# Kernel tuning notes

Measured on AMD Instinct MI355X. Metric: run time of the kernel, lower is better.

## Reference

```python
import jax, jax.numpy as jnp
import numpy as np

B, N_IN, O, IN_L, OUT_L = 256, 1152, 10, 8, 16
ITERS = 3
EPS = 1e-7

def squash(s, eps):
    # norm over the capsule-length axis (-2), keepdim, as in the torch code
    dot = jnp.sum(s * s, axis=-2, keepdims=True)
    return (dot / (1.0 + dot) / jnp.sqrt(dot + eps)) * s

def setup_inputs() -> dict:
    key = jax.random.key(0)
    k1, k2, k3 = jax.random.split(key, 3)
    x = jax.random.normal(k1, (B, N_IN, IN_L, 1), dtype=jnp.float32)
    weight = 0.05 * jax.random.normal(k2, (1, N_IN, O, IN_L, OUT_L), dtype=jnp.float32)
    bias = 0.05 * jax.random.normal(k3, (1, 1, O, OUT_L, 1), dtype=jnp.float32)
    return {"x": x, "weight": weight, "bias": bias}

def reference(x, weight, bias):
    # u_hat[b,n,o,k] = sum_i W[0,n,o,i,k] * x[b,n,i,0]  -> (B, N, O, K, 1)
    u_hat = jnp.einsum('noik,bni->bnok', weight[0], x[..., 0])[..., None]
    u_det = jax.lax.stop_gradient(u_hat)
    b_ij = jnp.zeros((x.shape[0], N_IN, O, 1, 1), dtype=x.dtype)
    v = None
    for r in range(ITERS):
        c = jax.nn.softmax(b_ij, axis=2)          # routing coefficients over out caps
        u = u_hat if r == ITERS - 1 else u_det    # detached except last iter
        s = jnp.sum(c * u, axis=1, keepdims=True) + bias  # (B,1,O,K,1)
        v = squash(s, EPS)
        if r != ITERS - 1:
            # agreement: sum over capsule-length axis 3 -> (B,N,O,1,1)
            b_ij = b_ij + jnp.sum(u_det * v, axis=3, keepdims=True)
    return v
```

## Files before the change

kernel.cpp:

```cpp
#include <hip/hip_runtime.h>
#include <hip/hip_bf16.h>

#define BB   256
#define NIN  1152
#define OO   10
#define IL   8
#define OL   16
#define ROW  (OO*OL)
#define EPSQ 1e-7f

typedef unsigned short ushx8 __attribute__((ext_vector_type(8)));
typedef unsigned short ushx4 __attribute__((ext_vector_type(4)));

__device__ __forceinline__ float bf2f(unsigned short h) {
    unsigned u = ((unsigned)h) << 16;
    return __builtin_bit_cast(float, u);
}

__global__ __launch_bounds__(320, 1) void caps_build(
    const float* __restrict__ x, const float* __restrict__ w,
    unsigned short* __restrict__ u)
{
    const int t  = threadIdx.x;
    const int nl = t / 20;
    const int s  = t - nl * 20;
    const int o  = s >> 1;
    const int k8 = s & 1;
    const int n  = blockIdx.x * 16 + nl;
    const int b0 = blockIdx.y * 32;

    const float* wb = w + (size_t)n * (OO * IL * OL) + (o * IL) * OL + k8 * 8;
    float wr[IL][8];
    #pragma unroll
    for (int i = 0; i < IL; ++i) {
        const float4 wa = *reinterpret_cast<const float4*>(wb + i * OL);
        const float4 wc = *reinterpret_cast<const float4*>(wb + i * OL + 4);
        wr[i][0] = wa.x; wr[i][1] = wa.y; wr[i][2] = wa.z; wr[i][3] = wa.w;
        wr[i][4] = wc.x; wr[i][5] = wc.y; wr[i][6] = wc.z; wr[i][7] = wc.w;
    }

    const float4* xb = reinterpret_cast<const float4*>(x + ((size_t)b0 * NIN + n) * IL);
    unsigned short* ub = u + ((size_t)b0 * NIN + n) * ROW + o * OL + k8 * 8;

    #pragma unroll 4
    for (int bl = 0; bl < 32; ++bl) {
        const float4 xa = xb[(size_t)bl * (NIN * 2)];
        const float4 xc = xb[(size_t)bl * (NIN * 2) + 1];
        const float xv[IL] = {xa.x, xa.y, xa.z, xa.w, xc.x, xc.y, xc.z, xc.w};

        float uv[8];
        #pragma unroll
        for (int j = 0; j < 8; ++j) {
            float acc = wr[0][j] * xv[0];
            #pragma unroll
            for (int i = 1; i < IL; ++i) acc = fmaf(wr[i][j], xv[i], acc);
            uv[j] = acc;
        }

        union { ushx8 v; __hip_bfloat162 h[4]; } pk;
        #pragma unroll
        for (int j = 0; j < 4; ++j)
            pk.h[j] = __float22bfloat162_rn(make_float2(uv[2 * j], uv[2 * j + 1]));
        *reinterpret_cast<ushx8*>(ub + (size_t)bl * ((size_t)NIN * ROW)) = pk.v;
    }
}

__global__ __launch_bounds__(512) void caps_route(
    const unsigned short* __restrict__ u, const float* __restrict__ vsum,
    const float* __restrict__ bias, const float* __restrict__ prevAdd,
    float* __restrict__ outv, float scale)
{
    __shared__ float lds[8][ROW];
    const int t = threadIdx.x;
    const int q = t & 3;
    const int g = t >> 2;
    const int b = blockIdx.x;
    const int wv = t >> 6;

    float4 sp[OO];
    #pragma unroll
    for (int o = 0; o < OO; ++o) sp[o] = make_float4(0.f, 0.f, 0.f, 0.f);

    const unsigned short* ub = u + (size_t)b * NIN * ROW + (q << 2);

    if (vsum == nullptr) {
        for (int m = 0; m < 9; ++m) {
            const unsigned short* un = ub + (size_t)(g + (m << 7)) * ROW;
            #pragma unroll
            for (int o = 0; o < OO; ++o) {
                const ushx4 raw = *reinterpret_cast<const ushx4*>(un + o * OL);
                sp[o].x += bf2f(raw[0]);
                sp[o].y += bf2f(raw[1]);
                sp[o].z += bf2f(raw[2]);
                sp[o].w += bf2f(raw[3]);
            }
        }
    } else {
        float4 vs[OO];
        #pragma unroll
        for (int o = 0; o < OO; ++o)
            vs[o] = *reinterpret_cast<const float4*>(vsum + (size_t)b * ROW + o * OL + q * 4);

        for (int m = 0; m < 9; ++m) {
            const unsigned short* un = ub + (size_t)(g + (m << 7)) * ROW;
            ushx4 raw[OO];
            #pragma unroll
            for (int o = 0; o < OO; ++o)
                raw[o] = *reinterpret_cast<const ushx4*>(un + o * OL);

            float bij[OO];
            #pragma unroll
            for (int o = 0; o < OO; ++o) {
                float d = bf2f(raw[o][0]) * vs[o].x;
                d = fmaf(bf2f(raw[o][1]), vs[o].y, d);
                d = fmaf(bf2f(raw[o][2]), vs[o].z, d);
                d = fmaf(bf2f(raw[o][3]), vs[o].w, d);
                d += __shfl_xor(d, 1, 4);
                d += __shfl_xor(d, 2, 4);
                bij[o] = d;
            }
            float mx = bij[0];
            #pragma unroll
            for (int o = 1; o < OO; ++o) mx = fmaxf(mx, bij[o]);
            float e[OO], se = 0.f;
            #pragma unroll
            for (int o = 0; o < OO; ++o) { e[o] = __expf(bij[o] - mx); se += e[o]; }
            const float r = 1.f / se;
            #pragma unroll
            for (int o = 0; o < OO; ++o) {
                const float c = e[o] * r;
                sp[o].x = fmaf(c, bf2f(raw[o][0]), sp[o].x);
                sp[o].y = fmaf(c, bf2f(raw[o][1]), sp[o].y);
                sp[o].z = fmaf(c, bf2f(raw[o][2]), sp[o].z);
                sp[o].w = fmaf(c, bf2f(raw[o][3]), sp[o].w);
            }
        }
    }

    #pragma unroll
    for (int o = 0; o < OO; ++o) {
        #pragma unroll
        for (int msk = 4; msk <= 32; msk <<= 1) {
            sp[o].x += __shfl_xor(sp[o].x, msk);
            sp[o].y += __shfl_xor(sp[o].y, msk);
            sp[o].z += __shfl_xor(sp[o].z, msk);
            sp[o].w += __shfl_xor(sp[o].w, msk);
        }
    }
    if ((t & 63) < 4) {
        #pragma unroll
        for (int o = 0; o < OO; ++o) {
            lds[wv][o * OL + q * 4 + 0] = sp[o].x;
            lds[wv][o * OL + q * 4 + 1] = sp[o].y;
            lds[wv][o * OL + q * 4 + 2] = sp[o].z;
            lds[wv][o * OL + q * 4 + 3] = sp[o].w;
        }
    }
    __syncthreads();

    if (t < ROW) {
        float ssum = 0.f;
        #pragma unroll
        for (int wvi = 0; wvi < 8; ++wvi) ssum += lds[wvi][t];
        const float sv = scale * ssum + bias[t];

        float d = sv * sv;
        d += __shfl_xor(d, 1, 16);
        d += __shfl_xor(d, 2, 16);
        d += __shfl_xor(d, 4, 16);
        d += __shfl_xor(d, 8, 16);
        const float f = d / ((1.f + d) * sqrtf(d + EPSQ));
        float v = f * sv;
        if (prevAdd) v += prevAdd[(size_t)b * ROW + t];
        outv[(size_t)b * ROW + t] = v;
    }
}

extern "C" void kernel_launch(void* const* d_in, const int* in_sizes, int n_in,
                              void* d_out, int out_size, void* d_ws, size_t ws_size,
                              hipStream_t stream) {
    const float* x    = (const float*)d_in[0];
    const float* w    = (const float*)d_in[1];
    const float* bias = (const float*)d_in[2];
    float* out = (float*)d_out;

    unsigned short* u = (unsigned short*)d_ws;
    float* v0  = (float*)((char*)d_ws + (size_t)BB * NIN * ROW * 2);
    float* vsb = v0 + (size_t)BB * ROW;

    caps_build<<<dim3(NIN / 16, BB / 32), 320, 0, stream>>>(x, w, u);
    caps_route<<<BB, 512, 0, stream>>>(u, nullptr, bias, nullptr, v0, 0.1f);
    caps_route<<<BB, 512, 0, stream>>>(u, v0, bias, v0, vsb, 1.0f);
    caps_route<<<BB, 512, 0, stream>>>(u, vsb, bias, nullptr, out, 1.0f);
}
```

Measured before the change: 92.36 us.

## Fuse three routing iterations into one kernel and stage build inputs in LDS

Replaces the three separate routing launches with a single 768-thread kernel per batch that loops over the iterations, keeping v in shared memory instead of round-tripping it through global memory. The build kernel now stages weights (with an XOR swizzle) and x tiles in LDS, uses smaller 8-capsule blocks, and computes two batch rows per step. This is meant to remove launch overhead and global v traffic, and to improve reuse in the build phase. In exchange it adds extra block-wide barriers and relies on the re-read of u across iterations being served by cache.

After: 87.58 us. 5.2% less time.

```diff
diff --git a/kernel.cpp b/kernel.cpp
--- a/kernel.cpp
+++ b/kernel.cpp
@@ -8,6 +8,8 @@
 #define OL   16
 #define ROW  (OO*OL)
 #define EPSQ 1e-7f
+#define NT   8
+#define BT   32
 
 typedef unsigned short ushx8 __attribute__((ext_vector_type(8)));
 typedef unsigned short ushx4 __attribute__((ext_vector_type(4)));
@@ -17,162 +19,195 @@
     return __builtin_bit_cast(float, u);
 }
 
-__global__ __launch_bounds__(320, 1) void caps_build(
+__global__ __launch_bounds__(160) void caps_build(
     const float* __restrict__ x, const float* __restrict__ w,
     unsigned short* __restrict__ u)
 {
+    __shared__ float4 wl4[NT][321];
+    __shared__ float4 xl4[BT * 16];
     const int t  = threadIdx.x;
+    const int n0 = blockIdx.x * NT;
+    const int b0 = blockIdx.y * BT;
+
+    const float4* wg = reinterpret_cast<const float4*>(w) + (size_t)n0 * 320;
+    for (int j = t; j < NT * 320; j += 160) {
+        const int row = j / 320;
+        const int lin = j - row * 320;
+        const int o   = lin >> 5;
+        const int rem = lin & 31;
+        const int i   = rem >> 2;
+        const int kh  = rem & 3;
+        const int ip  = i ^ (o & 1);
+        wl4[row][(o << 5) | (ip << 2) | kh] = wg[j];
+    }
+    const float4* xg = reinterpret_cast<const float4*>(x);
+    for (int j = t; j < BT * 16; j += 160) {
+        const int bl = j >> 4;
+        const int r  = j & 15;
+        xl4[j] = xg[((size_t)(b0 + bl) * NIN + n0) * 2 + r];
+    }
+    __syncthreads();
+
     const int nl = t / 20;
     const int s  = t - nl * 20;
     const int o  = s >> 1;
     const int k8 = s & 1;
-    const int n  = blockIdx.x * 16 + nl;
-    const int b0 = blockIdx.y * 32;
-
-    const float* wb = w + (size_t)n * (OO * IL * OL) + (o * IL) * OL + k8 * 8;
-    float wr[IL][8];
+    const int p  = o & 1;
+    const float4* wbase = &wl4[nl][(o << 5) | (k8 << 1)];
+    const float4* xbase = &xl4[nl * 2];
+    unsigned short* ub = u + ((size_t)b0 * NIN + n0 + nl) * ROW + o * OL + k8 * 8;
+    const size_t ustride = (size_t)NIN * ROW;
+
+    for (int bl = 0; bl < BT; bl += 2) {
+        const float4 xa0 = xbase[bl * 16];
+        const float4 xa1 = xbase[bl * 16 + 1];
+        const float4 xb0 = xbase[bl * 16 + 16];
+        const float4 xb1 = xbase[bl * 16 + 17];
+        const float xv0[IL] = {xa0.x, xa0.y, xa0.z, xa0.w, xa1.x, xa1.y, xa1.z, xa1.w};
+        const float xv1[IL] = {xb0.x, xb0.y, xb0.z, xb0.w, xb1.x, xb1.y, xb1.z, xb1.w};
+
+        float a0[8] = {0,0,0,0,0,0,0,0};
+        float a1[8] = {0,0,0,0,0,0,0,0};
+        #pragma unroll
+        for (int i = 0; i < IL; ++i) {
+            const float4 wlo = wbase[(i ^ p) << 2];
+            const float4 whi = wbase[((i ^ p) << 2) | 1];
+            const float wv[8] = {wlo.x, wlo.y, wlo.z, wlo.w, whi.x, whi.y, whi.z, whi.w};
+            #pragma unroll
+            for (int j = 0; j < 8; ++j) {
+                a0[j] = fmaf(wv[j], xv0[i], a0[j]);
+                a1[j] = fmaf(wv[j], xv1[i], a1[j]);
+            }
+        }
+        union { ushx8 v; __hip_bfloat162 h[4]; } p0, p1;
+        #pragma unroll
+        for (int j = 0; j < 4; ++j) {
+            p0.h[j] = __float22bfloat162_rn(make_float2(a0[2*j], a0[2*j+1]));
+            p1.h[j] = __float22bfloat162_rn(make_float2(a1[2*j], a1[2*j+1]));
+        }
+        *reinterpret_cast<ushx8*>(ub + (size_t)bl * ustride)       = p0.v;
+        *reinterpret_cast<ushx8*>(ub + (size_t)(bl + 1) * ustride) = p1.v;
+    }
+}
+
+__global__ __launch_bounds__(768) void caps_route3(
+    const unsigned short* __restrict__ u, const float* __restrict__ bias,
+    float* __restrict__ outv)
+{
+    __shared__ float lds[12][ROW];
+    __shared__ float vbuf[ROW];
+    const int t  = threadIdx.x;
+    const int q  = t & 3;
+    const int g  = t >> 2;
+    const int wv = t >> 6;
+    const int b  = blockIdx.x;
+    const unsigned short* ub = u + (size_t)b * NIN * ROW + (q << 2);
+
+    float bsv = 0.f;
+    if (t < ROW) bsv = bias[t];
+    float vprev = 0.f;
+
+    float4 sp[OO];
+
     #pragma unroll
-    for (int i = 0; i < IL; ++i) {
-        const float4 wa = *reinterpret_cast<const float4*>(wb + i * OL);
-        const float4 wc = *reinterpret_cast<const float4*>(wb + i * OL + 4);
-        wr[i][0] = wa.x; wr[i][1] = wa.y; wr[i][2] = wa.z; wr[i][3] = wa.w;
-        wr[i][4] = wc.x; wr[i][5] = wc.y; wr[i][6] = wc.z; wr[i][7] = wc.w;
-    }
-
-    const float4* xb = reinterpret_cast<const float4*>(x + ((size_t)b0 * NIN + n) * IL);
-    unsigned short* ub = u + ((size_t)b0 * NIN + n) * ROW + o * OL + k8 * 8;
-
-    #pragma unroll 4
-    for (int bl = 0; bl < 32; ++bl) {
-        const float4 xa = xb[(size_t)bl * (NIN * 2)];
-        const float4 xc = xb[(size_t)bl * (NIN * 2) + 1];
-        const float xv[IL] = {xa.x, xa.y, xa.z, xa.w, xc.x, xc.y, xc.z, xc.w};
-
-        float uv[8];
-        #pragma unroll
-        for (int j = 0; j < 8; ++j) {
-            float acc = wr[0][j] * xv[0];
-            #pragma unroll
-            for (int i = 1; i < IL; ++i) acc = fmaf(wr[i][j], xv[i], acc);
-            uv[j] = acc;
-        }
-
-        union { ushx8 v; __hip_bfloat162 h[4]; } pk;
-        #pragma unroll
-        for (int j = 0; j < 4; ++j)
-            pk.h[j] = __float22bfloat162_rn(make_float2(uv[2 * j], uv[2 * j + 1]));
-        *reinterpret_cast<ushx8*>(ub + (size_t)bl * ((size_t)NIN * ROW)) = pk.v;
-    }
-}
-
-__global__ __launch_bounds__(512) void caps_route(
-    const unsigned short* __restrict__ u, const float* __restrict__ vsum,
-    const float* __restrict__ bias, const float* __restrict__ prevAdd,
-    float* __restrict__ outv, float scale)
-{
-    __shared__ float lds[8][ROW];
-    const int t = threadIdx.x;
-    const int q = t & 3;
-    const int g = t >> 2;
-    const int b = blockIdx.x;
-    const int wv = t >> 6;
-
-    float4 sp[OO];
-    #pragma unroll
-    for (int o = 0; o < OO; ++o) sp[o] = make_float4(0.f, 0.f, 0.f, 0.f);
-
-    const unsigned short* ub = u + (size_t)b * NIN * ROW + (q << 2);
-
-    if (vsum == nullptr) {
-        for (int m = 0; m < 9; ++m) {
-            const unsigned short* un = ub + (size_t)(g + (m << 7)) * ROW;
+    for (int iter = 0; iter < 3; ++iter) {
+        #pragma unroll
+        for (int o = 0; o < OO; ++o) sp[o] = make_float4(0.f, 0.f, 0.f, 0.f);
+
+        if (iter == 0) {
+            for (int m = 0; m < 6; ++m) {
+                const unsigned short* un = ub + (size_t)(g + m * 192) * ROW;
+                #pragma unroll
+                for (int o = 0; o < OO; ++o) {
+                    const ushx4 raw = *reinterpret_cast<const ushx4*>(un + o * OL);
+                    sp[o].x += bf2f(raw[0]);
+                    sp[o].y += bf2f(raw[1]);
+                    sp[o].z += bf2f(raw[2]);
+                    sp[o].w += bf2f(raw[3]);
+                }
+            }
+        } else {
+            float4 vs[OO];
+            #pragma unroll
+            for (int o = 0; o < OO; ++o)
+                vs[o] = *reinterpret_cast<const float4*>(&vbuf[o * OL + (q << 2)]);
+
+            for (int m = 0; m < 6; ++m) {
+                const unsigned short* un = ub + (size_t)(g + m * 192) * ROW;
+                ushx4 raw[OO];
+                #pragma unroll
+                for (int o = 0; o < OO; ++o)
+                    raw[o] = *reinterpret_cast<const ushx4*>(un + o * OL);
+
+                float bij[OO];
+                #pragma unroll
+                for (int o = 0; o < OO; ++o) {
+                    float d = bf2f(raw[o][0]) * vs[o].x;
+                    d = fmaf(bf2f(raw[o][1]), vs[o].y, d);
+                    d = fmaf(bf2f(raw[o][2]), vs[o].z, d);
+                    d = fmaf(bf2f(raw[o][3]), vs[o].w, d);
+                    d += __shfl_xor(d, 1, 4);
+                    d += __shfl_xor(d, 2, 4);
+                    bij[o] = d;
+                }
+                float mx = bij[0];
+                #pragma unroll
+                for (int o = 1; o < OO; ++o) mx = fmaxf(mx, bij[o]);
+                float e[OO], se = 0.f;
+                #pragma unroll
+                for (int o = 0; o < OO; ++o) { e[o] = __expf(bij[o] - mx); se += e[o]; }
+                const float r = 1.f / se;
+                #pragma unroll
+                for (int o = 0; o < OO; ++o) {
+                    const float c = e[o] * r;
+                    sp[o].x = fmaf(c, bf2f(raw[o][0]), sp[o].x);
+                    sp[o].y = fmaf(c, bf2f(raw[o][1]), sp[o].y);
+                    sp[o].z = fmaf(c, bf2f(raw[o][2]), sp[o].z);
+                    sp[o].w = fmaf(c, bf2f(raw[o][3]), sp[o].w);
+                }
+            }
+        }
+
+        #pragma unroll
+        for (int o = 0; o < OO; ++o) {
+            #pragma unroll
+            for (int msk = 4; msk <= 32; msk <<= 1) {
+                sp[o].x += __shfl_xor(sp[o].x, msk);
+                sp[o].y += __shfl_xor(sp[o].y, msk);
+                sp[o].z += __shfl_xor(sp[o].z, msk);
+                sp[o].w += __shfl_xor(sp[o].w, msk);
+            }
+        }
+        if ((t & 63) < 4) {
             #pragma unroll
             for (int o = 0; o < OO; ++o) {
-                const ushx4 raw = *reinterpret_cast<const ushx4*>(un + o * OL);
-                sp[o].x += bf2f(raw[0]);
-                sp[o].y += bf2f(raw[1]);
-                sp[o].z += bf2f(raw[2]);
-                sp[o].w += bf2f(raw[3]);
-            }
-        }
-    } else {
-        float4 vs[OO];
-        #pragma unroll
-        for (int o = 0; o < OO; ++o)
-            vs[o] = *reinterpret_cast<const float4*>(vsum + (size_t)b * ROW + o * OL + q * 4);
-
-        for (int m = 0; m < 9; ++m) {
-            const unsigned short* un = ub + (size_t)(g + (m << 7)) * ROW;
-            ushx4 raw[OO];
-            #pragma unroll
-            for (int o = 0; o < OO; ++o)
-                raw[o] = *reinterpret_cast<const ushx4*>(un + o * OL);
-
-            float bij[OO];
-            #pragma unroll
-            for (int o = 0; o < OO; ++o) {
-                float d = bf2f(raw[o][0]) * vs[o].x;
-                d = fmaf(bf2f(raw[o][1]), vs[o].y, d);
-                d = fmaf(bf2f(raw[o][2]), vs[o].z, d);
-                d = fmaf(bf2f(raw[o][3]), vs[o].w, d);
-                d += __shfl_xor(d, 1, 4);
-                d += __shfl_xor(d, 2, 4);
-                bij[o] = d;
-            }
-            float mx = bij[0];
-            #pragma unroll
-            for (int o = 1; o < OO; ++o) mx = fmaxf(mx, bij[o]);
-            float e[OO], se = 0.f;
-            #pragma unroll
-            for (int o = 0; o < OO; ++o) { e[o] = __expf(bij[o] - mx); se += e[o]; }
-            const float r = 1.f / se;
-            #pragma unroll
-            for (int o = 0; o < OO; ++o) {
-                const float c = e[o] * r;
-                sp[o].x = fmaf(c, bf2f(raw[o][0]), sp[o].x);
-                sp[o].y = fmaf(c, bf2f(raw[o][1]), sp[o].y);
-                sp[o].z = fmaf(c, bf2f(raw[o][2]), sp[o].z);
-                sp[o].w = fmaf(c, bf2f(raw[o][3]), sp[o].w);
-            }
-        }
-    }
-
-    #pragma unroll
-    for (int o = 0; o < OO; ++o) {
-        #pragma unroll
-        for (int msk = 4; msk <= 32; msk <<= 1) {
-            sp[o].x += __shfl_xor(sp[o].x, msk);
-            sp[o].y += __shfl_xor(sp[o].y, msk);
-            sp[o].z += __shfl_xor(sp[o].z, msk);
-            sp[o].w += __shfl_xor(sp[o].w, msk);
-        }
-    }
-    if ((t & 63) < 4) {
-        #pragma unroll
-        for (int o = 0; o < OO; ++o) {
-            lds[wv][o * OL + q * 4 + 0] = sp[o].x;
-            lds[wv][o * OL + q * 4 + 1] = sp[o].y;
-            lds[wv][o * OL + q * 4 + 2] = sp[o].z;
-            lds[wv][o * OL + q * 4 + 3] = sp[o].w;
-        }
-    }
-    __syncthreads();
-
-    if (t < ROW) {
-        float ssum = 0.f;
-        #pragma unroll
-        for (int wvi = 0; wvi < 8; ++wvi) ssum += lds[wvi][t];
-        const float sv = scale * ssum + bias[t];
-
-        float d = sv * sv;
-        d += __shfl_xor(d, 1, 16);
-        d += __shfl_xor(d, 2, 16);
-        d += __shfl_xor(d, 4, 16);
-        d += __shfl_xor(d, 8, 16);
-        const float f = d / ((1.f + d) * sqrtf(d + EPSQ));
-        float v = f * sv;
-        if (prevAdd) v += prevAdd[(size_t)b * ROW + t];
-        outv[(size_t)b * ROW + t] = v;
+                lds[wv][o * OL + q * 4 + 0] = sp[o].x;
+                lds[wv][o * OL + q * 4 + 1] = sp[o].y;
+                lds[wv][o * OL + q * 4 + 2] = sp[o].z;
+                lds[wv][o * OL + q * 4 + 3] = sp[o].w;
+            }
+        }
+        __syncthreads();
+
+        if (t < ROW) {
+            float ssum = 0.f;
+            #pragma unroll
+            for (int wvi = 0; wvi < 12; ++wvi) ssum += lds[wvi][t];
+            const float sv = (iter == 0 ? 0.1f : 1.0f) * ssum + bsv;
+
+            float d = sv * sv;
+            d += __shfl_xor(d, 1, 16);
+            d += __shfl_xor(d, 2, 16);
+            d += __shfl_xor(d, 4, 16);
+            d += __shfl_xor(d, 8, 16);
+            const float f = d / ((1.f + d) * sqrtf(d + EPSQ));
+            const float v = f * sv;
+
+            if (iter == 0) { vbuf[t] = v; vprev = v; }
+            else if (iter == 1) { vbuf[t] = v + vprev; }
+            else { outv[(size_t)b * ROW + t] = v; }
+        }
+        __syncthreads();
     }
 }
 
@@ -185,11 +220,7 @@
     float* out = (float*)d_out;
 
     unsigned short* u = (unsigned short*)d_ws;
-    float* v0  = (float*)((char*)d_ws + (size_t)BB * NIN * ROW * 2);
-    float* vsb = v0 + (size_t)BB * ROW;
-
-    caps_build<<<dim3(NIN / 16, BB / 32), 320, 0, stream>>>(x, w, u);
-    caps_route<<<BB, 512, 0, stream>>>(u, nullptr, bias, nullptr, v0, 0.1f);
-    caps_route<<<BB, 512, 0, stream>>>(u, v0, bias, v0, vsb, 1.0f);
-    caps_route<<<BB, 512, 0, stream>>>(u, vsb, bias, nullptr, out, 1.0f);
-}
+
+    caps_build<<<dim3(NIN / NT, BB / BT), 160, 0, stream>>>(x, w, u);
+    caps_route3<<<BB, 768, 0, stream>>>(u, bias, out);
+}
```
